# Kernel tuning notes

Hardware: AMD Instinct MI355X
Metric: run time of the kernel (lower is better)

The kernel has to match this reference:

```python
import jax, jax.numpy as jnp
import numpy as np

NUM_HEADS = 16

def setup_inputs() -> dict:
    key = jax.random.key(0)
    ks = jax.random.split(key, 6)
    B_, N, C = 1024, 64, 512
    nW = 256
    s = 0.02
    return {
        "x": jax.random.normal(ks[0], (B_, N, C), jnp.float32),
        "mask": jax.random.normal(ks[1], (nW, N, N), jnp.float32),
        "Wq": jax.random.normal(ks[2], (C, C), jnp.float32) * s,
        "bq": jnp.zeros((C,), jnp.float32),
        "Wkv": jax.random.normal(ks[3], (C, 2 * C), jnp.float32) * s,
        "bkv": jnp.zeros((2 * C,), jnp.float32),
        "Wp": jax.random.normal(ks[4], (C, C), jnp.float32) * s,
        "bp": jnp.zeros((C,), jnp.float32),
    }

def reference(x, mask, Wq, bq, Wkv, bkv, Wp, bp):
    B_, N, C = x.shape
    H = NUM_HEADS
    D = C // H
    scale = D ** -0.5
    # QKV projections (self-attention: attn_kv is x)
    q = (x @ Wq + bq).reshape(B_, N, H, D).transpose(0, 2, 1, 3)   # [B,H,N,D]
    kv = (x @ Wkv + bkv).reshape(B_, N, 2, H, D).transpose(2, 0, 3, 1, 4)
    k, v = kv[0], kv[1]                                            # [B,H,N,D]
    attn = jnp.einsum('bhnd,bhmd->bhnm', q * scale, k)             # [B,H,N,N]
    nW = mask.shape[0]
    # add window mask: [B//nW, nW, H, N, N] + [1, nW, 1, N, N]
    attn = attn.reshape(B_ // nW, nW, H, N, N) + mask[None, :, None, :, :]
    attn = jax.nn.softmax(attn.reshape(B_, H, N, N), axis=-1)
    out = jnp.einsum('bhnm,bhmd->bhnd', attn, v)                   # [B,H,N,D]
    out = out.transpose(0, 2, 1, 3).reshape(B_, N, C)
    return out @ Wp + bp
```

## Files before the change

kernel.cpp:

```cpp
#include <hip/hip_runtime.h>
#include <hip/hip_bf16.h>
#include <stdint.h>

typedef float f32x4 __attribute__((ext_vector_type(4)));
typedef short s16x8 __attribute__((ext_vector_type(8)));
typedef short s16x4 __attribute__((ext_vector_type(4)));

__device__ __forceinline__ f32x4 mfma16(s16x8 a, s16x8 b, f32x4 c) {
  return __builtin_amdgcn_mfma_f32_16x16x32_bf16(a, b, c, 0, 0, 0);
}

typedef __attribute__((address_space(3))) void lds_void;
typedef const __attribute__((address_space(1))) void gbl_void;

__device__ __forceinline__ void gload_lds16(const void* g, void* l) {
  __builtin_amdgcn_global_load_lds((gbl_void*)g, (lds_void*)l, 16, 0, 0);
}

__device__ __forceinline__ short f2bf(float f) {
  uint32_t u = __builtin_bit_cast(uint32_t, f);
  u += 0x7fffu + ((u >> 16) & 1u);
  return (short)(u >> 16);
}

__global__ __launch_bounds__(256) void k_cvt_x(const float* __restrict__ in,
                                               short* __restrict__ out) {
  const int i = blockIdx.x * 256 + threadIdx.x;
  const f32x4 v = ((const f32x4*)in)[i];
  s16x4 o;
  o[0] = f2bf(v[0]); o[1] = f2bf(v[1]); o[2] = f2bf(v[2]); o[3] = f2bf(v[3]);
  ((s16x4*)out)[i] = o;
}

__global__ __launch_bounds__(256) void k_transpose_w(const float* __restrict__ W,
                                                     short* __restrict__ Wt,
                                                     int K, int N) {
  __shared__ float tile[32][33];
  const int nb = blockIdx.x * 32;
  const int kb = blockIdx.y * 32;
  const int tx = threadIdx.x & 31;
  const int ty = threadIdx.x >> 5;
#pragma unroll
  for (int r = 0; r < 4; ++r)
    tile[ty + 8 * r][tx] = W[(size_t)(kb + ty + 8 * r) * N + nb + tx];
  __syncthreads();
#pragma unroll
  for (int r = 0; r < 4; ++r)
    Wt[(size_t)(nb + ty + 8 * r) * K + kb + tx] = f2bf(tile[tx][ty + 8 * r]);
}

__device__ __forceinline__ void gemm_mainloop_512(const short* __restrict__ Ag,
                                                  const short* __restrict__ Bg,
                                                  f32x4 acc[4][4]) {
  __shared__ char smem[65536];
  const int t = threadIdx.x;
  const int lane = t & 63;
  const int wv = t >> 6;
  const int lg = lane >> 4;
  const int l15 = lane & 15;
  const int wr = wv >> 1;
  const int wc = wv & 1;

#define STAGE_TILE(slot, kt)                                                  \
  {                                                                           \
    char* base_ = smem + (slot) * 32768;                                      \
    _Pragma("unroll") for (int i_ = 0; i_ < 4; ++i_) {                        \
      const int p_ = (i_ * 256 + t) * 16;                                     \
      const int row_ = p_ >> 7;                                               \
      const int kb_ = (p_ & 127) ^ ((row_ & 7) << 4);                         \
      gload_lds16((const char*)Ag + (size_t)row_ * 1024 + (kt) * 128 + kb_,   \
                  base_ + i_ * 4096 + wv * 1024);                             \
      gload_lds16((const char*)Bg + (size_t)row_ * 1024 + (kt) * 128 + kb_,   \
                  base_ + 16384 + i_ * 4096 + wv * 1024);                     \
    }                                                                         \
  }

  STAGE_TILE(0, 0);
  __syncthreads();

  for (int kt = 0; kt < 8; ++kt) {
    const int s = kt & 1;
    if (kt < 7) STAGE_TILE(s ^ 1, kt + 1);
    const char* As = smem + s * 32768;
    const char* Bs = As + 16384;
#pragma unroll
    for (int ks = 0; ks < 2; ++ks) {
      s16x8 a[4], b[4];
#pragma unroll
      for (int f = 0; f < 4; ++f) {
        const int ra = wr * 64 + f * 16 + l15;
        a[f] = *(const s16x8*)(As + ra * 128 +
                               ((ks * 64 + lg * 16) ^ ((ra & 7) << 4)));
      }
#pragma unroll
      for (int f = 0; f < 4; ++f) {
        const int rb = wc * 64 + f * 16 + l15;
        b[f] = *(const s16x8*)(Bs + rb * 128 +
                               ((ks * 64 + lg * 16) ^ ((rb & 7) << 4)));
      }
#pragma unroll
      for (int fm = 0; fm < 4; ++fm)
#pragma unroll
        for (int fn = 0; fn < 4; ++fn)
          acc[fm][fn] = mfma16(a[fm], b[fn], acc[fm][fn]);
    }
    __syncthreads();
  }
#undef STAGE_TILE
}

__global__ __launch_bounds__(256) void k_gemm_qkv(
    const short* __restrict__ xb, const short* __restrict__ Wqt,
    const short* __restrict__ Wkvt, const float* __restrict__ bq,
    const float* __restrict__ bkv, short* __restrict__ Qb,
    short* __restrict__ Kb, short* __restrict__ Vb) {
  const int bid = blockIdx.x;
  const int orig = (bid & 7) * 768 + (bid >> 3);
  const int bm = orig / 12;
  const int bn = orig % 12;
  f32x4 acc[4][4];
  const f32x4 z = {0.f, 0.f, 0.f, 0.f};
  for (int i = 0; i < 4; ++i)
    for (int j = 0; j < 4; ++j) acc[i][j] = z;

  const short* Ag = xb + (size_t)bm * 128 * 512;
  const short* Bg = (bn < 4) ? (Wqt + (size_t)bn * 128 * 512)
                             : (Wkvt + (size_t)(bn - 4) * 128 * 512);
  gemm_mainloop_512(Ag, Bg, acc);

  const int t = threadIdx.x, lane = t & 63, wv = t >> 6;
  const int lg = lane >> 4, l15 = lane & 15;
  const int wr = wv >> 1, wc = wv & 1;
  const int m0 = bm * 128 + wr * 64;
  const int n0 = bn * 128 + wc * 64;

  short* dst; int nsub; const float* bias; int bsub;
  if (bn < 4)      { dst = Qb; nsub = 0;    bias = bq;  bsub = 0; }
  else if (bn < 8) { dst = Kb; nsub = 512;  bias = bkv; bsub = 512; }
  else             { dst = Vb; nsub = 1024; bias = bkv; bsub = 512; }

#pragma unroll
  for (int fm = 0; fm < 4; ++fm)
#pragma unroll
    for (int fn = 0; fn < 4; ++fn)
#pragma unroll
      for (int j = 0; j < 4; ++j) {
        const int m = m0 + fm * 16 + lg * 4 + j;
        const int n = n0 + fn * 16 + l15;
        const float v = acc[fm][fn][j] + bias[n - bsub];
        const int c = n - nsub;
        const int h = c >> 5, d = c & 31;
        const int b = m >> 6, nr = m & 63;
        dst[((size_t)(b * 16 + h) * 64 + nr) * 32 + d] = f2bf(v);
      }
}

__global__ __launch_bounds__(256) void k_attn(
    const short* __restrict__ Qb, const short* __restrict__ Kb,
    const short* __restrict__ Vb, const float* __restrict__ mask,
    short* __restrict__ AO) {
  __shared__ char vt[4096];
  __shared__ char pb[8192];
  const int gid = blockIdx.x;
  const int b = gid >> 4, h = gid & 15;
  const int t = threadIdx.x, lane = t & 63, wv = t >> 6;
  const int lg = lane >> 4, l15 = lane & 15;
  const short* qg = Qb + (size_t)gid * 2048;
  const short* kg = Kb + (size_t)gid * 2048;
  const short* vg = Vb + (size_t)gid * 2048;

  {
    const s16x8 vv = *(const s16x8*)(vg + t * 8);
    const int m = t >> 2, d0 = (t & 3) * 8;
#pragma unroll
    for (int j = 0; j < 8; ++j) {
      const int d = d0 + j;
      *(short*)(vt + d * 128 + ((2 * m) ^ ((d & 7) << 4))) = vv[j];
    }
  }

  const s16x8 qf = *(const s16x8*)(qg + (wv * 16 + l15) * 32 + lg * 8);
  f32x4 s[4];
  const f32x4 z = {0.f, 0.f, 0.f, 0.f};
#pragma unroll
  for (int fn = 0; fn < 4; ++fn) {
    const s16x8 kf = *(const s16x8*)(kg + (fn * 16 + l15) * 32 + lg * 8);
    s[fn] = mfma16(qf, kf, z);
  }

  const float scale = 0.17677669529663687f;
  const float* mrow = mask + (size_t)(b & 255) * 4096;
  float sv[4][4];
#pragma unroll
  for (int fn = 0; fn < 4; ++fn)
#pragma unroll
    for (int j = 0; j < 4; ++j)
      sv[fn][j] = s[fn][j] * scale +
                  mrow[(wv * 16 + lg * 4 + j) * 64 + fn * 16 + l15];
#pragma unroll
  for (int j = 0; j < 4; ++j) {
    float mx = fmaxf(fmaxf(sv[0][j], sv[1][j]), fmaxf(sv[2][j], sv[3][j]));
#pragma unroll
    for (int off = 1; off < 16; off <<= 1) mx = fmaxf(mx, __shfl_xor(mx, off));
    float sum = 0.f;
#pragma unroll
    for (int fn = 0; fn < 4; ++fn) {
      sv[fn][j] = __expf(sv[fn][j] - mx);
      sum += sv[fn][j];
    }
#pragma unroll
    for (int off = 1; off < 16; off <<= 1) sum += __shfl_xor(sum, off);
    const float inv = 1.f / sum;
#pragma unroll
    for (int fn = 0; fn < 4; ++fn) sv[fn][j] *= inv;
  }

  char* pw = pb + wv * 2048;
#pragma unroll
  for (int fn = 0; fn < 4; ++fn)
#pragma unroll
    for (int j = 0; j < 4; ++j) {
      const int row = lg * 4 + j;
      const int col = fn * 16 + l15;
      *(short*)(pw + row * 128 + ((col * 2) ^ ((row & 7) << 4))) =
          f2bf(sv[fn][j]);
    }

  __syncthreads();

  f32x4 o[2];
  o[0] = z; o[1] = z;
#pragma unroll
  for (int ks = 0; ks < 2; ++ks) {
    const s16x8 pa = *(const s16x8*)(pw + l15 * 128 +
                                     ((ks * 64 + lg * 16) ^ ((l15 & 7) << 4)));
#pragma unroll
    for (int fd = 0; fd < 2; ++fd) {
      const int d = fd * 16 + l15;
      const s16x8 vb = *(const s16x8*)(vt + d * 128 +
                                       ((ks * 64 + lg * 16) ^ ((d & 7) << 4)));
      o[fd] = mfma16(pa, vb, o[fd]);
    }
  }

#pragma unroll
  for (int fd = 0; fd < 2; ++fd)
#pragma unroll
    for (int j = 0; j < 4; ++j) {
      const int row = wv * 16 + lg * 4 + j;
      const int d = fd * 16 + l15;
      AO[((size_t)(b * 64 + row)) * 512 + h * 32 + d] = f2bf(o[fd][j]);
    }
}

__global__ __launch_bounds__(256) void k_gemm_proj(
    const short* __restrict__ AO, const short* __restrict__ Wpt,
    const float* __restrict__ bp, float* __restrict__ out) {
  const int bid = blockIdx.x;
  const int orig = (bid & 7) * 256 + (bid >> 3);
  const int bm = orig >> 2;
  const int bn = orig & 3;
  f32x4 acc[4][4];
  const f32x4 z = {0.f, 0.f, 0.f, 0.f};
  for (int i = 0; i < 4; ++i)
    for (int j = 0; j < 4; ++j) acc[i][j] = z;

  gemm_mainloop_512(AO + (size_t)bm * 65536, Wpt + (size_t)bn * 65536, acc);

  const int t = threadIdx.x, lane = t & 63, wv = t >> 6;
  const int lg = lane >> 4, l15 = lane & 15;
  const int wr = wv >> 1, wc = wv & 1;
  const int m0 = bm * 128 + wr * 64;
  const int n0 = bn * 128 + wc * 64;
#pragma unroll
  for (int fm = 0; fm < 4; ++fm)
#pragma unroll
    for (int fn = 0; fn < 4; ++fn)
#pragma unroll
      for (int j = 0; j < 4; ++j) {
        const int m = m0 + fm * 16 + lg * 4 + j;
        const int n = n0 + fn * 16 + l15;
        out[(size_t)m * 512 + n] = acc[fm][fn][j] + bp[n];
      }
}

extern "C" void kernel_launch(void* const* d_in, const int* in_sizes, int n_in,
                              void* d_out, int out_size, void* d_ws,
                              size_t ws_size, hipStream_t stream) {
  const float* x    = (const float*)d_in[0];
  const float* mask = (const float*)d_in[1];
  const float* Wq   = (const float*)d_in[2];
  const float* bq   = (const float*)d_in[3];
  const float* Wkv  = (const float*)d_in[4];
  const float* bkv  = (const float*)d_in[5];
  const float* Wp   = (const float*)d_in[6];
  const float* bp   = (const float*)d_in[7];
  float* out = (float*)d_out;
  char* ws = (char*)d_ws;

  short* xb   = (short*)(ws);
  short* Wqt  = (short*)(ws + 67108864);
  short* Wkvt = (short*)(ws + 67108864 + 524288);
  short* Wpt  = (short*)(ws + 67108864 + 1572864);
  short* Qb   = (short*)(ws + 69206016);
  short* Kb   = (short*)(ws + 69206016 + 67108864);
  short* Vb   = (short*)(ws + 69206016 + 2 * 67108864);
  short* AO   = xb;

  k_cvt_x<<<dim3(32768), dim3(256), 0, stream>>>(x, xb);
  k_transpose_w<<<dim3(16, 16), dim3(256), 0, stream>>>(Wq, Wqt, 512, 512);
  k_transpose_w<<<dim3(32, 16), dim3(256), 0, stream>>>(Wkv, Wkvt, 512, 1024);
  k_transpose_w<<<dim3(16, 16), dim3(256), 0, stream>>>(Wp, Wpt, 512, 512);
  k_gemm_qkv<<<dim3(6144), dim3(256), 0, stream>>>(xb, Wqt, Wkvt, bq, bkv,
                                                   Qb, Kb, Vb);
  k_attn<<<dim3(16384), dim3(256), 0, stream>>>(Qb, Kb, Vb, mask, AO);
  k_gemm_proj<<<dim3(2048), dim3(256), 0, stream>>>(AO, Wpt, bp, out);
}
```

Before: 492.2 us.

## Fuse QKV projection GEMM with per-head windowed attention in one kernel

Result: slower. 531.7 us (+8.0%).

```diff
diff --git a/kernel.cpp b/kernel.cpp
--- a/kernel.cpp
+++ b/kernel.cpp
@@ -109,148 +109,207 @@
 #undef STAGE_TILE
 }
 
-__global__ __launch_bounds__(256) void k_gemm_qkv(
+__global__ __launch_bounds__(256) void k_qkv_attn(
     const short* __restrict__ xb, const short* __restrict__ Wqt,
     const short* __restrict__ Wkvt, const float* __restrict__ bq,
-    const float* __restrict__ bkv, short* __restrict__ Qb,
-    short* __restrict__ Kb, short* __restrict__ Vb) {
+    const float* __restrict__ bkv, const float* __restrict__ mask,
+    short* __restrict__ AO) {
+  __shared__ char smem[57344];
   const int bid = blockIdx.x;
-  const int orig = (bid & 7) * 768 + (bid >> 3);
-  const int bm = orig / 12;
-  const int bn = orig % 12;
-  f32x4 acc[4][4];
-  const f32x4 z = {0.f, 0.f, 0.f, 0.f};
-  for (int i = 0; i < 4; ++i)
-    for (int j = 0; j < 4; ++j) acc[i][j] = z;
-
-  const short* Ag = xb + (size_t)bm * 128 * 512;
-  const short* Bg = (bn < 4) ? (Wqt + (size_t)bn * 128 * 512)
-                             : (Wkvt + (size_t)(bn - 4) * 128 * 512);
-  gemm_mainloop_512(Ag, Bg, acc);
-
+  const int orig = (bid & 7) * 1024 + (bid >> 3);
+  const int bm = orig >> 4;
+  const int h = orig & 15;
   const int t = threadIdx.x, lane = t & 63, wv = t >> 6;
   const int lg = lane >> 4, l15 = lane & 15;
   const int wr = wv >> 1, wc = wv & 1;
-  const int m0 = bm * 128 + wr * 64;
-  const int n0 = bn * 128 + wc * 64;
-
-  short* dst; int nsub; const float* bias; int bsub;
-  if (bn < 4)      { dst = Qb; nsub = 0;    bias = bq;  bsub = 0; }
-  else if (bn < 8) { dst = Kb; nsub = 512;  bias = bkv; bsub = 512; }
-  else             { dst = Vb; nsub = 1024; bias = bkv; bsub = 512; }
-
+
+  const short* Ag = xb + (size_t)bm * 128 * 512;
+
+  f32x4 acc[4][3];
+  const f32x4 z = {0.f, 0.f, 0.f, 0.f};
+#pragma unroll
+  for (int i = 0; i < 4; ++i)
+#pragma unroll
+    for (int j = 0; j < 3; ++j) acc[i][j] = z;
+
+#define STAGE_QKV(slot, kt)                                                   \
+  {                                                                           \
+    char* base_ = smem + (slot) * 28672;                                      \
+    _Pragma("unroll") for (int i_ = 0; i_ < 4; ++i_) {                        \
+      const int p_ = (i_ * 256 + t) * 16;                                     \
+      const int row_ = p_ >> 7;                                               \
+      const int kb_ = (p_ & 127) ^ ((row_ & 7) << 4);                         \
+      gload_lds16((const char*)Ag + (size_t)row_ * 1024 + (kt) * 128 + kb_,   \
+                  base_ + i_ * 4096 + wv * 1024);                             \
+    }                                                                         \
+    _Pragma("unroll") for (int i_ = 0; i_ < 3; ++i_) {                        \
+      const int p_ = (i_ * 256 + t) * 16;                                     \
+      const int row_ = p_ >> 7;          \
+      const int ra_ = row_ - i_ * 32;                 \
+      const int kb_ = (p_ & 127) ^ ((row_ & 7) << 4);                         \
+      const short* br_ = (i_ == 0) ? Wqt + (size_t)(h * 32 + ra_) * 512       \
+                       : (i_ == 1) ? Wkvt + (size_t)(h * 32 + ra_) * 512      \
+                                   : Wkvt + (size_t)(512 + h * 32 + ra_) * 512;\
+      gload_lds16((const char*)br_ + (kt) * 128 + kb_,                        \
+                  base_ + 16384 + i_ * 4096 + wv * 1024);                     \
+    }                                                                         \
+  }
+
+  STAGE_QKV(0, 0);
+  __syncthreads();
+  for (int kt = 0; kt < 8; ++kt) {
+    const int s = kt & 1;
+    if (kt < 7) STAGE_QKV(s ^ 1, kt + 1);
+    const char* As = smem + s * 28672;
+    const char* Bs = As + 16384;
+#pragma unroll
+    for (int ks = 0; ks < 2; ++ks) {
+      s16x8 a[4], b[3];
+#pragma unroll
+      for (int f = 0; f < 4; ++f) {
+        const int ra = wr * 64 + f * 16 + l15;
+        a[f] = *(const s16x8*)(As + ra * 128 +
+                               ((ks * 64 + lg * 16) ^ ((ra & 7) << 4)));
+      }
+#pragma unroll
+      for (int f = 0; f < 3; ++f) {
+        const int rb = wc * 48 + f * 16 + l15;
+        b[f] = *(const s16x8*)(Bs + rb * 128 +
+                               ((ks * 64 + lg * 16) ^ ((rb & 7) << 4)));
+      }
+#pragma unroll
+      for (int fm = 0; fm < 4; ++fm)
+#pragma unroll
+        for (int fn = 0; fn < 3; ++fn)
+          acc[fm][fn] = mfma16(a[fm], b[fn], acc[fm][fn]);
+    }
+    __syncthreads();
+  }
+#undef STAGE_QKV
+
+  char* Qs = smem;
+  char* Ks = smem + 8192;
+  char* Vt = smem + 16384;
+  char* Pb = smem + 24576;
 #pragma unroll
   for (int fm = 0; fm < 4; ++fm)
 #pragma unroll
+    for (int fn = 0; fn < 3; ++fn)
+#pragma unroll
+      for (int j = 0; j < 4; ++j) {
+        const int m = wr * 64 + fm * 16 + lg * 4 + j;
+        const int c = wc * 48 + fn * 16 + l15;
+        float v = acc[fm][fn][j];
+        if (c < 32) {
+          v += bq[h * 32 + c];
+          *(short*)(Qs + m * 64 + (((c >> 3) ^ ((m >> 1) & 3)) << 4) +
+                    ((c & 7) * 2)) = f2bf(v);
+        } else if (c < 64) {
+          const int cc = c - 32;
+          v += bkv[h * 32 + cc];
+          *(short*)(Ks + m * 64 + (((cc >> 3) ^ ((m >> 1) & 3)) << 4) +
+                    ((cc & 7) * 2)) = f2bf(v);
+        } else {
+          const int cc = c - 64;
+          v += bkv[512 + h * 32 + cc];
+          *(short*)(Vt + (m >> 6) * 4096 + cc * 128 +
+                    (((m & 63) * 2) ^ ((cc & 7) << 4))) = f2bf(v);
+        }
+      }
+  __syncthreads();
+
+  const int wi = wv >> 1, rh = wv & 1;
+  const float* mrow = mask + (size_t)((2 * bm + wi) & 255) * 4096;
+
+  s16x8 qa[2];
+#pragma unroll
+  for (int fm = 0; fm < 2; ++fm) {
+    const int qr = wi * 64 + rh * 32 + fm * 16 + l15;
+    qa[fm] = *(const s16x8*)(Qs + qr * 64 + ((lg ^ ((qr >> 1) & 3)) << 4));
+  }
+  f32x4 sacc[2][4];
+#pragma unroll
+  for (int fn = 0; fn < 4; ++fn) {
+    const int kr = wi * 64 + fn * 16 + l15;
+    const s16x8 kf =
+        *(const s16x8*)(Ks + kr * 64 + ((lg ^ ((kr >> 1) & 3)) << 4));
+#pragma unroll
+    for (int fm = 0; fm < 2; ++fm) sacc[fm][fn] = mfma16(qa[fm], kf, z);
+  }
+
+  const float scale = 0.17677669529663687f;
+  float sv[2][4][4];
+#pragma unroll
+  for (int fm = 0; fm < 2; ++fm)
+#pragma unroll
     for (int fn = 0; fn < 4; ++fn)
 #pragma unroll
+      for (int j = 0; j < 4; ++j)
+        sv[fm][fn][j] = sacc[fm][fn][j] * scale +
+                        mrow[(rh * 32 + fm * 16 + lg * 4 + j) * 64 +
+                             fn * 16 + l15];
+#pragma unroll
+  for (int fm = 0; fm < 2; ++fm)
+#pragma unroll
+    for (int j = 0; j < 4; ++j) {
+      float mx = fmaxf(fmaxf(sv[fm][0][j], sv[fm][1][j]),
+                       fmaxf(sv[fm][2][j], sv[fm][3][j]));
+#pragma unroll
+      for (int off = 1; off < 16; off <<= 1) mx = fmaxf(mx, __shfl_xor(mx, off));
+      float sum = 0.f;
+#pragma unroll
+      for (int fn = 0; fn < 4; ++fn) {
+        sv[fm][fn][j] = __expf(sv[fm][fn][j] - mx);
+        sum += sv[fm][fn][j];
+      }
+#pragma unroll
+      for (int off = 1; off < 16; off <<= 1) sum += __shfl_xor(sum, off);
+      const float inv = 1.f / sum;
+#pragma unroll
+      for (int fn = 0; fn < 4; ++fn) sv[fm][fn][j] *= inv;
+    }
+
+  char* pw = Pb + wv * 4096;
+#pragma unroll
+  for (int fm = 0; fm < 2; ++fm)
+#pragma unroll
+    for (int fn = 0; fn < 4; ++fn)
+#pragma unroll
       for (int j = 0; j < 4; ++j) {
-        const int m = m0 + fm * 16 + lg * 4 + j;
-        const int n = n0 + fn * 16 + l15;
-        const float v = acc[fm][fn][j] + bias[n - bsub];
-        const int c = n - nsub;
-        const int h = c >> 5, d = c & 31;
-        const int b = m >> 6, nr = m & 63;
-        dst[((size_t)(b * 16 + h) * 64 + nr) * 32 + d] = f2bf(v);
-      }
-}
-
-__global__ __launch_bounds__(256) void k_attn(
-    const short* __restrict__ Qb, const short* __restrict__ Kb,
-    const short* __restrict__ Vb, const float* __restrict__ mask,
-    short* __restrict__ AO) {
-  __shared__ char vt[4096];
-  __shared__ char pb[8192];
-  const int gid = blockIdx.x;
-  const int b = gid >> 4, h = gid & 15;
-  const int t = threadIdx.x, lane = t & 63, wv = t >> 6;
-  const int lg = lane >> 4, l15 = lane & 15;
-  const short* qg = Qb + (size_t)gid * 2048;
-  const short* kg = Kb + (size_t)gid * 2048;
-  const short* vg = Vb + (size_t)gid * 2048;
-
-  {
-    const s16x8 vv = *(const s16x8*)(vg + t * 8);
-    const int m = t >> 2, d0 = (t & 3) * 8;
-#pragma unroll
-    for (int j = 0; j < 8; ++j) {
-      const int d = d0 + j;
-      *(short*)(vt + d * 128 + ((2 * m) ^ ((d & 7) << 4))) = vv[j];
+        const int prow = fm * 16 + lg * 4 + j;
+        const int pcol = fn * 16 + l15;
+        *(short*)(pw + prow * 128 + ((pcol * 2) ^ ((prow & 7) << 4))) =
+            f2bf(sv[fm][fn][j]);
+      }
+
+  f32x4 od[2][2];
+  od[0][0] = z; od[0][1] = z; od[1][0] = z; od[1][1] = z;
+#pragma unroll
+  for (int ks = 0; ks < 2; ++ks) {
+#pragma unroll
+    for (int fm = 0; fm < 2; ++fm) {
+      const s16x8 pa = *(const s16x8*)(pw + (fm * 16 + l15) * 128 +
+                                       ((ks * 64 + lg * 16) ^ ((l15 & 7) << 4)));
+#pragma unroll
+      for (int fd = 0; fd < 2; ++fd) {
+        const int d = fd * 16 + l15;
+        const s16x8 vb = *(const s16x8*)(Vt + wi * 4096 + d * 128 +
+                                         ((ks * 64 + lg * 16) ^ ((d & 7) << 4)));
+        od[fm][fd] = mfma16(pa, vb, od[fm][fd]);
+      }
     }
   }
 
-  const s16x8 qf = *(const s16x8*)(qg + (wv * 16 + l15) * 32 + lg * 8);
-  f32x4 s[4];
-  const f32x4 z = {0.f, 0.f, 0.f, 0.f};
-#pragma unroll
-  for (int fn = 0; fn < 4; ++fn) {
-    const s16x8 kf = *(const s16x8*)(kg + (fn * 16 + l15) * 32 + lg * 8);
-    s[fn] = mfma16(qf, kf, z);
-  }
-
-  const float scale = 0.17677669529663687f;
-  const float* mrow = mask + (size_t)(b & 255) * 4096;
-  float sv[4][4];
-#pragma unroll
-  for (int fn = 0; fn < 4; ++fn)
-#pragma unroll
-    for (int j = 0; j < 4; ++j)
-      sv[fn][j] = s[fn][j] * scale +
-                  mrow[(wv * 16 + lg * 4 + j) * 64 + fn * 16 + l15];
-#pragma unroll
-  for (int j = 0; j < 4; ++j) {
-    float mx = fmaxf(fmaxf(sv[0][j], sv[1][j]), fmaxf(sv[2][j], sv[3][j]));
-#pragma unroll
-    for (int off = 1; off < 16; off <<= 1) mx = fmaxf(mx, __shfl_xor(mx, off));
-    float sum = 0.f;
-#pragma unroll
-    for (int fn = 0; fn < 4; ++fn) {
-      sv[fn][j] = __expf(sv[fn][j] - mx);
-      sum += sv[fn][j];
-    }
-#pragma unroll
-    for (int off = 1; off < 16; off <<= 1) sum += __shfl_xor(sum, off);
-    const float inv = 1.f / sum;
-#pragma unroll
-    for (int fn = 0; fn < 4; ++fn) sv[fn][j] *= inv;
-  }
-
-  char* pw = pb + wv * 2048;
-#pragma unroll
-  for (int fn = 0; fn < 4; ++fn)
-#pragma unroll
-    for (int j = 0; j < 4; ++j) {
-      const int row = lg * 4 + j;
-      const int col = fn * 16 + l15;
-      *(short*)(pw + row * 128 + ((col * 2) ^ ((row & 7) << 4))) =
-          f2bf(sv[fn][j]);
-    }
-
-  __syncthreads();
-
-  f32x4 o[2];
-  o[0] = z; o[1] = z;
-#pragma unroll
-  for (int ks = 0; ks < 2; ++ks) {
-    const s16x8 pa = *(const s16x8*)(pw + l15 * 128 +
-                                     ((ks * 64 + lg * 16) ^ ((l15 & 7) << 4)));
-#pragma unroll
-    for (int fd = 0; fd < 2; ++fd) {
-      const int d = fd * 16 + l15;
-      const s16x8 vb = *(const s16x8*)(vt + d * 128 +
-                                       ((ks * 64 + lg * 16) ^ ((d & 7) << 4)));
-      o[fd] = mfma16(pa, vb, o[fd]);
-    }
-  }
-
-#pragma unroll
-  for (int fd = 0; fd < 2; ++fd)
-#pragma unroll
-    for (int j = 0; j < 4; ++j) {
-      const int row = wv * 16 + lg * 4 + j;
-      const int d = fd * 16 + l15;
-      AO[((size_t)(b * 64 + row)) * 512 + h * 32 + d] = f2bf(o[fd][j]);
-    }
+#pragma unroll
+  for (int fm = 0; fm < 2; ++fm)
+#pragma unroll
+    for (int fd = 0; fd < 2; ++fd)
+#pragma unroll
+      for (int j = 0; j < 4; ++j) {
+        const int row = bm * 128 + wi * 64 + rh * 32 + fm * 16 + lg * 4 + j;
+        const int col = h * 32 + fd * 16 + l15;
+        AO[(size_t)row * 512 + col] = f2bf(od[fm][fd][j]);
+      }
 }
 
 __global__ __launch_bounds__(256) void k_gemm_proj(
@@ -302,17 +361,13 @@
   short* Wqt  = (short*)(ws + 67108864);
   short* Wkvt = (short*)(ws + 67108864 + 524288);
   short* Wpt  = (short*)(ws + 67108864 + 1572864);
-  short* Qb   = (short*)(ws + 69206016);
-  short* Kb   = (short*)(ws + 69206016 + 67108864);
-  short* Vb   = (short*)(ws + 69206016 + 2 * 67108864);
-  short* AO   = xb;
+  short* AO   = (short*)(ws + 69206016);
 
   k_cvt_x<<<dim3(32768), dim3(256), 0, stream>>>(x, xb);
   k_transpose_w<<<dim3(16, 16), dim3(256), 0, stream>>>(Wq, Wqt, 512, 512);
   k_transpose_w<<<dim3(32, 16), dim3(256), 0, stream>>>(Wkv, Wkvt, 512, 1024);
   k_transpose_w<<<dim3(16, 16), dim3(256), 0, stream>>>(Wp, Wpt, 512, 512);
-  k_gemm_qkv<<<dim3(6144), dim3(256), 0, stream>>>(xb, Wqt, Wkvt, bq, bkv,
-                                                   Qb, Kb, Vb);
-  k_attn<<<dim3(16384), dim3(256), 0, stream>>>(Qb, Kb, Vb, mask, AO);
+  k_qkv_attn<<<dim3(8192), dim3(256), 0, stream>>>(xb, Wqt, Wkvt, bq, bkv,
+                                                   mask, AO);
   k_gemm_proj<<<dim3(2048), dim3(256), 0, stream>>>(AO, Wpt, bp, out);
 }
```
